# Performance work log

Measured on AMD Instinct MI355X. Metric: run time of the kernel, lower is better.

## Reference

```python
import jax, jax.numpy as jnp
import numpy as np

DIM = 1024
NUM_HEADS = 16
HEAD_DIM = DIM // NUM_HEADS


def setup_inputs() -> dict:
    key = jax.random.key(0)
    ks = jax.random.split(key, 9)
    s = 1.0 / np.sqrt(DIM)
    x = jax.random.normal(ks[0], (2, 2048, DIM), dtype=jnp.float32)
    Wq = jax.random.uniform(ks[1], (DIM, DIM), jnp.float32, -s, s)
    bq = jax.random.uniform(ks[2], (DIM,), jnp.float32, -s, s)
    Wk = jax.random.uniform(ks[3], (DIM, DIM), jnp.float32, -s, s)
    bk = jax.random.uniform(ks[4], (DIM,), jnp.float32, -s, s)
    Wv = jax.random.uniform(ks[5], (DIM, DIM), jnp.float32, -s, s)
    bv = jax.random.uniform(ks[6], (DIM,), jnp.float32, -s, s)
    Wo = jax.random.uniform(ks[7], (DIM, DIM), jnp.float32, -s, s)
    bo = jax.random.uniform(ks[8], (DIM,), jnp.float32, -s, s)
    return {"x": x, "Wq": Wq, "bq": bq, "Wk": Wk, "bk": bk,
            "Wv": Wv, "bv": bv, "Wo": Wo, "bo": bo}


def reference(x, Wq, bq, Wk, bk, Wv, bv, Wo, bo):
    B, S, _ = x.shape
    # projections (torch Linear: y = x @ W.T + b); split heads -> [B, H, S, Dh]
    def split(y):
        return y.reshape(B, S, NUM_HEADS, HEAD_DIM).transpose(0, 2, 1, 3)
    q = split(x @ Wq.T + bq)
    k = split(x @ Wk.T + bk)
    v = split(x @ Wv.T + bv)
    scale = 1.0 / np.sqrt(HEAD_DIM).astype(np.float32)
    scores = jnp.einsum('bhqd,bhkd->bhqk', q, k) * scale  # [B,H,S,S]
    attn = jax.nn.softmax(scores, axis=-1)
    ctx = jnp.einsum('bhqk,bhkd->bhqd', attn, v)  # [B,H,S,Dh]
    ctx = ctx.transpose(0, 2, 1, 3).reshape(B, S, DIM)
    return ctx @ Wo.T + bo
```

## Files before the change

kernel.cpp:

```cpp
#include <hip/hip_runtime.h>
#include <hip/hip_bf16.h>
#include <math.h>

#define DIMSZ 1024
#define NHEAD 16
#define HDIM 64
#define BATCH 2
#define SEQ 2048
#define NROWS (BATCH * SEQ)

#define QSCALE 0.18033688011112042592f

typedef __attribute__((ext_vector_type(8))) _Float16 f16x8;
typedef __attribute__((ext_vector_type(4))) float f32x4;

__device__ __forceinline__ int swz(int m) { return (m ^ (m >> 2)) & 3; }

__device__ __forceinline__ ushort f2h(float x) {
    union { _Float16 h; ushort u; } cv;
    cv.h = (_Float16)x;
    return cv.u;
}

__device__ __forceinline__ void gld16(const void* g, void* l) {
    __builtin_amdgcn_global_load_lds((const __attribute__((address_space(1))) void*)g,
                                     (__attribute__((address_space(3))) void*)l,
                                     16, 0, 0);
}

__global__ __launch_bounds__(256) void convert_all(
    const float* __restrict__ x,
    const float* __restrict__ Wq, const float* __restrict__ Wk,
    const float* __restrict__ Wv, const float* __restrict__ Wo,
    ushort* __restrict__ Xh, ushort* __restrict__ Wh, ushort* __restrict__ Woh)
{
    const int b = blockIdx.x;
    const float* src;
    ushort* dst;
    size_t off;
    if (b < 2048)      { src = x;  dst = Xh;             off = (size_t)b * 2048; }
    else if (b < 2560) { src = Wq; dst = Wh;             off = (size_t)(b - 2048) * 2048; }
    else if (b < 3072) { src = Wk; dst = Wh + (1 << 20); off = (size_t)(b - 2560) * 2048; }
    else if (b < 3584) { src = Wv; dst = Wh + 2 * (1 << 20); off = (size_t)(b - 3072) * 2048; }
    else               { src = Wo; dst = Woh;            off = (size_t)(b - 3584) * 2048; }

    const size_t i = off + (size_t)threadIdx.x * 8;
    const float4 f0 = *(const float4*)&src[i];
    const float4 f1 = *(const float4*)&src[i + 4];
    uint4 hv;
    hv.x = (unsigned)f2h(f0.x) | ((unsigned)f2h(f0.y) << 16);
    hv.y = (unsigned)f2h(f0.z) | ((unsigned)f2h(f0.w) << 16);
    hv.z = (unsigned)f2h(f1.x) | ((unsigned)f2h(f1.y) << 16);
    hv.w = (unsigned)f2h(f1.z) | ((unsigned)f2h(f1.w) << 16);
    *(uint4*)&dst[i] = hv;
}

__global__ __launch_bounds__(256, 3) void qkv_gemm(
    const ushort* __restrict__ Xh,
    const ushort* __restrict__ Wh,
    const float* __restrict__ bq, const float* __restrict__ bk,
    const float* __restrict__ bv,
    ushort* __restrict__ Qb, ushort* __restrict__ Kb, ushort* __restrict__ Vt)
{
    __shared__ __align__(16) ushort smem[17408];

    const int tid = threadIdx.x;
    const int wave = tid >> 6;
    const int lane = tid & 63;
    const int lm = lane & 15;
    const int lq = lane >> 4;
    const int wy = wave >> 1;
    const int wx = wave & 1;
    const int m0 = blockIdx.x * 128;
    const int nbase = blockIdx.y * 128;

    const int c = tid & 3;
    const int r0 = tid >> 2;
    const int g = c ^ swz(r0 & 15);
    const ushort* gah = Xh + (size_t)(m0 + r0) * DIMSZ + g * 8;
    const ushort* gbh = Wh + (size_t)(nbase + r0) * DIMSZ + g * 8;
    const int wofs = wave * 512;

    const int fo = lm * 32 + (((lq ^ swz(lm)) & 3) << 3);
    int aofs[4], bofs[4];
#pragma unroll
    for (int i = 0; i < 4; ++i) {
        aofs[i] = (wy * 64 + i * 16) * 32 + fo;
        bofs[i] = (wx * 64 + i * 16) * 32 + fo;
    }

    f32x4 acc[4][4] = {};

    {
        gld16(gah, smem + wofs);                 gld16(gah + 64 * DIMSZ, smem + 2048 + wofs);
        gld16(gbh, smem + 4096 + wofs);          gld16(gbh + 64 * DIMSZ, smem + 6144 + wofs);
    }

    for (int kk = 0; kk < 32; ++kk) {
        __syncthreads();

        const ushort* Ah = smem;
        const ushort* Bh = smem + 4096;

        f16x8 ahf[4], bhf[4];
#pragma unroll
        for (int i = 0; i < 4; ++i) {
            ahf[i] = *(const f16x8*)&Ah[aofs[i]];
            bhf[i] = *(const f16x8*)&Bh[bofs[i]];
        }

        __syncthreads();

        if (kk + 1 < 32) {
            const int k0 = (kk + 1) * 32;
            gld16(gah + k0, smem + wofs);                 gld16(gah + 64 * DIMSZ + k0, smem + 2048 + wofs);
            gld16(gbh + k0, smem + 4096 + wofs);          gld16(gbh + 64 * DIMSZ + k0, smem + 6144 + wofs);
        }

#pragma unroll
        for (int i = 0; i < 4; ++i)
#pragma unroll
            for (int j = 0; j < 4; ++j)
                acc[i][j] = __builtin_amdgcn_mfma_f32_16x16x32_f16(ahf[i], bhf[j], acc[i][j], 0, 0, 0);
    }

    const int mat = blockIdx.y >> 3;
    const float* bias = (mat == 0) ? bq : (mat == 1) ? bk : bv;
    const int nloc0 = (blockIdx.y & 7) * 128;
    const int b = m0 >> 11;
    const int s0 = m0 & (SEQ - 1);
    ushort* sf = smem;

    __syncthreads();

    if (mat == 2) {
#pragma unroll
        for (int j = 0; j < 4; ++j) {
            const int nc = nloc0 + wx * 64 + j * 16 + lm;
            const float bb = bias[nc];
            const int d = j * 16 + lm;
#pragma unroll
            for (int i = 0; i < 4; ++i) {
                const int ss = wy * 64 + (i >> 1) * 32 + lq * 8 + (i & 1) * 4;
                ushort4 pk;
                pk.x = f2h(acc[i][j][0] + bb);
                pk.y = f2h(acc[i][j][1] + bb);
                pk.z = f2h(acc[i][j][2] + bb);
                pk.w = f2h(acc[i][j][3] + bb);
                *(ushort4*)&sf[(wx * 64 + d) * 136 + ss] = pk;
            }
        }
        __syncthreads();
#pragma unroll
        for (int p = 0; p < 8; ++p) {
            const int idx = p * 256 + tid;
            const int row = idx >> 4;
            const int hh = row >> 6;
            const int d = row & 63;
            const int sseg = (idx & 15) * 8;
            const uint4 v = *(const uint4*)&sf[row * 136 + sseg];
            const int hg = (nloc0 >> 6) + hh;
            *(uint4*)&Vt[((size_t)(b * NHEAD + hg) * HDIM + d) * SEQ + s0 + sseg] = v;
        }
    } else {
        ushort* dst = (mat == 0) ? Qb : Kb;
        const float sc = (mat == 0) ? QSCALE : 1.0f;
#pragma unroll
        for (int j = 0; j < 4; ++j) {
            const int col = wx * 64 + j * 16 + lm;
            const float bb = bias[nloc0 + col];
#pragma unroll
            for (int i = 0; i < 4; ++i) {
                const int rbase = wy * 64 + i * 16 + lq * 4;
#pragma unroll
                for (int rr = 0; rr < 4; ++rr)
                    sf[(rbase + rr) * 136 + col] = f2h((acc[i][j][rr] + bb) * sc);
            }
        }
        __syncthreads();
#pragma unroll
        for (int p = 0; p < 8; ++p) {
            const int idx = p * 256 + tid;
            const int row = idx >> 4;
            const int seg = idx & 15;
            const uint4 v = *(const uint4*)&sf[row * 136 + seg * 8];
            const int nc0 = nloc0 + seg * 8;
            const int h = nc0 >> 6;
            const int d = nc0 & 63;
            *(uint4*)&dst[((size_t)(b * NHEAD + h) * SEQ + s0 + row) * HDIM + d] = v;
        }
    }
}

__global__ __launch_bounds__(512, 4) void flash_attn_mfma(
    const ushort* __restrict__ Qb, const ushort* __restrict__ Kb,
    const ushort* __restrict__ Vt, ushort* __restrict__ CTXh)
{
    __shared__ __align__(16) ushort Ks[2][4096];
    __shared__ __align__(16) ushort Vs[2][4096];

    const int tid = threadIdx.x;
    const int w = tid >> 6;
    const int l = tid & 63;
    const int lm = l & 15;
    const int lq = l >> 4;
    const int q0 = blockIdx.x * 128;
    const int bh = blockIdx.y;

    const ushort* Kg = Kb + (size_t)bh * SEQ * HDIM;
    const ushort* Vg = Vt + (size_t)bh * HDIM * SEQ;

    const int srow = w * 8 + (l >> 3);
    const int sc_ = (l & 7) ^ ((l >> 3) & 7);

    f16x8 qf[2];
#pragma unroll
    for (int kt = 0; kt < 2; ++kt)
        qf[kt] = *(const f16x8*)&Qb[((size_t)bh * SEQ + q0 + w * 16 + lm) * HDIM + kt * 32 + lq * 8];

    int koff[4][2];
#pragma unroll
    for (int t = 0; t < 4; ++t)
#pragma unroll
        for (int kt = 0; kt < 2; ++kt)
            koff[t][kt] = (t * 16 + lm) * 64 + (((kt * 4 + lq) ^ (lm & 7)) << 3);

    f32x4 o[4] = {};
    float l_ = 0.0f;

    gld16(Kg + (size_t)srow * HDIM + sc_ * 8, &Ks[0][0] + w * 8 * 64);
    gld16(Vg + (size_t)srow * SEQ + sc_ * 8, &Vs[0][0] + w * 8 * 64);

    for (int ch = 0; ch < SEQ / 64; ++ch) {
        __syncthreads();

        if (ch + 1 < SEQ / 64) {
            const int kc = (ch + 1) * 64;
            ushort* kb_n = &Ks[(ch + 1) & 1][0];
            ushort* vb_n = &Vs[(ch + 1) & 1][0];
            gld16(Kg + (size_t)(kc + srow) * HDIM + sc_ * 8, kb_n + w * 8 * 64);
            gld16(Vg + (size_t)srow * SEQ + kc + sc_ * 8, vb_n + w * 8 * 64);
        }

        const ushort* kb = &Ks[ch & 1][0];
        const ushort* vb = &Vs[ch & 1][0];

        f32x4 st[4] = {};
#pragma unroll
        for (int ct = 0; ct < 4; ++ct)
#pragma unroll
            for (int kt = 0; kt < 2; ++kt) {
                const f16x8 kf = *(const f16x8*)&kb[koff[ct][kt]];
                st[ct] = __builtin_amdgcn_mfma_f32_16x16x32_f16(kf, qf[kt], st[ct], 0, 0, 0);
            }

        {
            float ls = 0.0f;
#pragma unroll
            for (int ct = 0; ct < 4; ++ct)
#pragma unroll
                for (int r = 0; r < 4; ++r) {
                    const float p = __builtin_amdgcn_exp2f(st[ct][r]);
                    st[ct][r] = p;
                    ls += p;
                }
            ls += __shfl_xor(ls, 16, 64);
            ls += __shfl_xor(ls, 32, 64);
            l_ += ls;
        }

        f16x8 pf[2];
#pragma unroll
        for (int kt2 = 0; kt2 < 2; ++kt2) {
            union { f16x8 v; ushort u[8]; } pk;
#pragma unroll
            for (int t = 0; t < 2; ++t)
#pragma unroll
                for (int r = 0; r < 4; ++r)
                    pk.u[t * 4 + r] = f2h(st[kt2 * 2 + t][r]);
            pf[kt2] = pk.v;
        }

#pragma unroll
        for (int dt = 0; dt < 4; ++dt)
#pragma unroll
            for (int kt2 = 0; kt2 < 2; ++kt2) {
                const f16x8 vf = *(const f16x8*)&vb[koff[dt][kt2]];
                o[dt] = __builtin_amdgcn_mfma_f32_16x16x32_f16(pf[kt2], vf, o[dt], 0, 0, 0);
            }
    }

    const int b = bh >> 4;
    const int h = bh & 15;
    const float linv_me = 1.0f / l_;
#pragma unroll
    for (int r = 0; r < 4; ++r) {
        const float lr = __shfl(linv_me, lq * 4 + r, 64);
        const int srow_ = q0 + w * 16 + lq * 4 + r;
        const size_t base = ((size_t)b * SEQ + srow_) * DIMSZ + h * HDIM;
#pragma unroll
        for (int dt = 0; dt < 4; ++dt)
            CTXh[base + dt * 16 + lm] = f2h(o[dt][r] * lr);
    }
}

__global__ __launch_bounds__(256) void oproj_gemm(
    const ushort* __restrict__ Ah_g, const ushort* __restrict__ Bh_g,
    const float* __restrict__ bias, float* __restrict__ out)
{
    __shared__ __align__(16) ushort smem[6144];

    const int tid = threadIdx.x;
    const int wave = tid >> 6;
    const int lane = tid & 63;
    const int lm = lane & 15;
    const int lq = lane >> 4;
    const int wy = wave >> 1;
    const int wx = wave & 1;
    const int m0 = blockIdx.x * 64;
    const int n0 = blockIdx.y * 128;

    const int c = tid & 3;
    const int r0 = tid >> 2;
    const int g = c ^ swz(r0 & 15);
    const ushort* gah = Ah_g + (size_t)(m0 + r0) * DIMSZ + g * 8;
    const ushort* gbh = Bh_g + (size_t)(n0 + r0) * DIMSZ + g * 8;
    const int wofs = wave * 512;

    const int fo = lm * 32 + (((lq ^ swz(lm)) & 3) << 3);
    int aofs[2], bofs[4];
#pragma unroll
    for (int i = 0; i < 2; ++i) aofs[i] = (wy * 32 + i * 16) * 32 + fo;
#pragma unroll
    for (int j = 0; j < 4; ++j) bofs[j] = (wx * 64 + j * 16) * 32 + fo;

    f32x4 acc[2][4] = {};

    {
        gld16(gah, smem + wofs);
        gld16(gbh, smem + 2048 + wofs);   gld16(gbh + 64 * DIMSZ, smem + 4096 + wofs);
    }

    for (int kk = 0; kk < 32; ++kk) {
        __syncthreads();

        f16x8 ahf[2], bhf[4];
#pragma unroll
        for (int i = 0; i < 2; ++i) ahf[i] = *(const f16x8*)&smem[aofs[i]];
#pragma unroll
        for (int j = 0; j < 4; ++j) bhf[j] = *(const f16x8*)&smem[2048 + bofs[j]];

        __syncthreads();

        if (kk + 1 < 32) {
            const int k0 = (kk + 1) * 32;
            gld16(gah + k0, smem + wofs);
            gld16(gbh + k0, smem + 2048 + wofs);   gld16(gbh + 64 * DIMSZ + k0, smem + 4096 + wofs);
        }

#pragma unroll
        for (int i = 0; i < 2; ++i)
#pragma unroll
            for (int j = 0; j < 4; ++j)
                acc[i][j] = __builtin_amdgcn_mfma_f32_16x16x32_f16(ahf[i], bhf[j], acc[i][j], 0, 0, 0);
    }

#pragma unroll
    for (int j = 0; j < 4; ++j) {
        const int nc = n0 + wx * 64 + j * 16 + lm;
        const float bb = bias[nc];
#pragma unroll
        for (int i = 0; i < 2; ++i) {
            const int mb = m0 + wy * 32 + i * 16 + lq * 4;
#pragma unroll
            for (int rr = 0; rr < 4; ++rr)
                out[(size_t)(mb + rr) * DIMSZ + nc] = acc[i][j][rr] + bb;
        }
    }
}

extern "C" void kernel_launch(void* const* d_in, const int* in_sizes, int n_in,
                              void* d_out, int out_size, void* d_ws, size_t ws_size,
                              hipStream_t stream)
{
    const float* x  = (const float*)d_in[0];
    const float* Wq = (const float*)d_in[1];
    const float* bq = (const float*)d_in[2];
    const float* Wk = (const float*)d_in[3];
    const float* bk = (const float*)d_in[4];
    const float* Wv = (const float*)d_in[5];
    const float* bv = (const float*)d_in[6];
    const float* Wo = (const float*)d_in[7];
    const float* bo = (const float*)d_in[8];
    float* out = (float*)d_out;

    const size_t elems = (size_t)NROWS * DIMSZ;
    ushort* Qb   = (ushort*)d_ws;
    ushort* Kb   = Qb + elems;
    ushort* Vt   = Kb + elems;
    ushort* CTXh = Vt + elems;
    ushort* Wh   = CTXh + elems;
    ushort* Woh  = Wh + 3 * (1 << 20);
    ushort* Xh   = CTXh;

    convert_all<<<4096, 256, 0, stream>>>(x, Wq, Wk, Wv, Wo, Xh, Wh, Woh);

    qkv_gemm<<<dim3(32, 24), 256, 0, stream>>>(Xh, Wh, bq, bk, bv, Qb, Kb, Vt);

    flash_attn_mfma<<<dim3(SEQ / 128, BATCH * NHEAD), 512, 0, stream>>>(Qb, Kb, Vt, CTXh);

    oproj_gemm<<<dim3(64, 8), 256, 0, stream>>>(CTXh, Woh, bo, out);
}
```

Before: 182.4 us.

## Double KV chunk to 128, compute softmax denominator via MFMA, use packed cvt

The flash attention kernel now processes 128-key chunks per iteration instead of 64, which halves the number of barriers and loop iterations, and doubles the LDS buffers. The row-sum of probabilities is computed with an MFMA against a ones vector rather than with per-lane adds and cross-lane shuffles. Float-to-half conversion uses the packed round-toward-zero convert. This trades higher LDS use (64KB per block), which may limit occupancy under the 4-blocks launch bound, for fewer synchronisations and less VALU work. Round-toward-zero slightly changes rounding, and the denominator is now summed from the fp16-rounded probabilities.

```diff
diff --git a/kernel.cpp b/kernel.cpp
--- a/kernel.cpp
+++ b/kernel.cpp
@@ -12,6 +12,7 @@
 #define QSCALE 0.18033688011112042592f
 
 typedef __attribute__((ext_vector_type(8))) _Float16 f16x8;
+typedef __attribute__((ext_vector_type(2))) __fp16 fp16x2;
 typedef __attribute__((ext_vector_type(4))) float f32x4;
 
 __device__ __forceinline__ int swz(int m) { return (m ^ (m >> 2)) & 3; }
@@ -20,6 +21,12 @@
     union { _Float16 h; ushort u; } cv;
     cv.h = (_Float16)x;
     return cv.u;
+}
+
+__device__ __forceinline__ unsigned pkrtz(float a, float b) {
+    union { fp16x2 v; unsigned u; } c;
+    c.v = __builtin_amdgcn_cvt_pkrtz(a, b);
+    return c.u;
 }
 
 __device__ __forceinline__ void gld16(const void* g, void* l) {
@@ -196,8 +203,8 @@
     const ushort* __restrict__ Qb, const ushort* __restrict__ Kb,
     const ushort* __restrict__ Vt, ushort* __restrict__ CTXh)
 {
-    __shared__ __align__(16) ushort Ks[2][4096];
-    __shared__ __align__(16) ushort Vs[2][4096];
+    __shared__ __align__(16) ushort Ks[2][8192];
+    __shared__ __align__(16) ushort Vs[2][8192];
 
     const int tid = threadIdx.x;
     const int w = tid >> 6;
@@ -210,92 +217,99 @@
     const ushort* Kg = Kb + (size_t)bh * SEQ * HDIM;
     const ushort* Vg = Vt + (size_t)bh * HDIM * SEQ;
 
-    const int srow = w * 8 + (l >> 3);
-    const int sc_ = (l & 7) ^ ((l >> 3) & 7);
+    const int krow_ = w * 8 + (l >> 3);
+    const int kg_ = (l & 7) ^ ((l >> 3) & 7);
+    const int vrow_ = w * 4 + (l >> 4);
+    const int vg_ = (l & 15) ^ (vrow_ & 7);
 
     f16x8 qf[2];
 #pragma unroll
     for (int kt = 0; kt < 2; ++kt)
         qf[kt] = *(const f16x8*)&Qb[((size_t)bh * SEQ + q0 + w * 16 + lm) * HDIM + kt * 32 + lq * 8];
 
-    int koff[4][2];
-#pragma unroll
-    for (int t = 0; t < 4; ++t)
-#pragma unroll
-        for (int kt = 0; kt < 2; ++kt)
-            koff[t][kt] = (t * 16 + lm) * 64 + (((kt * 4 + lq) ^ (lm & 7)) << 3);
+    int kbase[2], vbase[4];
+#pragma unroll
+    for (int kt = 0; kt < 2; ++kt)
+        kbase[kt] = lm * 64 + (((kt * 4 + lq) ^ (lm & 7)) << 3);
+#pragma unroll
+    for (int kt2 = 0; kt2 < 4; ++kt2)
+        vbase[kt2] = lm * 128 + (((kt2 * 4 + lq) ^ (lm & 7)) << 3);
+
+    f16x8 vones;
+#pragma unroll
+    for (int i = 0; i < 8; ++i) vones[i] = (_Float16)1.0f;
 
     f32x4 o[4] = {};
-    float l_ = 0.0f;
-
-    gld16(Kg + (size_t)srow * HDIM + sc_ * 8, &Ks[0][0] + w * 8 * 64);
-    gld16(Vg + (size_t)srow * SEQ + sc_ * 8, &Vs[0][0] + w * 8 * 64);
-
-    for (int ch = 0; ch < SEQ / 64; ++ch) {
-        __syncthreads();
-
-        if (ch + 1 < SEQ / 64) {
-            const int kc = (ch + 1) * 64;
+    f32x4 lacc = {};
+
+#pragma unroll
+    for (int p = 0; p < 2; ++p) {
+        gld16(Kg + (size_t)(p * 64 + krow_) * HDIM + kg_ * 8, &Ks[0][0] + (p * 64 + w * 8) * 64);
+        gld16(Vg + (size_t)(p * 32 + vrow_) * SEQ + vg_ * 8, &Vs[0][0] + (p * 32 + w * 4) * 128);
+    }
+
+    for (int ch = 0; ch < SEQ / 128; ++ch) {
+        __syncthreads();
+
+        if (ch + 1 < SEQ / 128) {
+            const int kc = (ch + 1) * 128;
             ushort* kb_n = &Ks[(ch + 1) & 1][0];
             ushort* vb_n = &Vs[(ch + 1) & 1][0];
-            gld16(Kg + (size_t)(kc + srow) * HDIM + sc_ * 8, kb_n + w * 8 * 64);
-            gld16(Vg + (size_t)srow * SEQ + kc + sc_ * 8, vb_n + w * 8 * 64);
+#pragma unroll
+            for (int p = 0; p < 2; ++p) {
+                gld16(Kg + (size_t)(kc + p * 64 + krow_) * HDIM + kg_ * 8, kb_n + (p * 64 + w * 8) * 64);
+                gld16(Vg + (size_t)(p * 32 + vrow_) * SEQ + kc + vg_ * 8, vb_n + (p * 32 + w * 4) * 128);
+            }
         }
 
         const ushort* kb = &Ks[ch & 1][0];
         const ushort* vb = &Vs[ch & 1][0];
 
-        f32x4 st[4] = {};
-#pragma unroll
-        for (int ct = 0; ct < 4; ++ct)
+        f32x4 st[8] = {};
+#pragma unroll
+        for (int ct = 0; ct < 8; ++ct)
 #pragma unroll
             for (int kt = 0; kt < 2; ++kt) {
-                const f16x8 kf = *(const f16x8*)&kb[koff[ct][kt]];
+                const f16x8 kf = *(const f16x8*)&kb[ct * 1024 + kbase[kt]];
                 st[ct] = __builtin_amdgcn_mfma_f32_16x16x32_f16(kf, qf[kt], st[ct], 0, 0, 0);
             }
 
-        {
-            float ls = 0.0f;
-#pragma unroll
-            for (int ct = 0; ct < 4; ++ct)
-#pragma unroll
-                for (int r = 0; r < 4; ++r) {
-                    const float p = __builtin_amdgcn_exp2f(st[ct][r]);
-                    st[ct][r] = p;
-                    ls += p;
-                }
-            ls += __shfl_xor(ls, 16, 64);
-            ls += __shfl_xor(ls, 32, 64);
-            l_ += ls;
-        }
-
-        f16x8 pf[2];
-#pragma unroll
-        for (int kt2 = 0; kt2 < 2; ++kt2) {
-            union { f16x8 v; ushort u[8]; } pk;
-#pragma unroll
-            for (int t = 0; t < 2; ++t)
-#pragma unroll
-                for (int r = 0; r < 4; ++r)
-                    pk.u[t * 4 + r] = f2h(st[kt2 * 2 + t][r]);
+#pragma unroll
+        for (int ct = 0; ct < 8; ++ct)
+#pragma unroll
+            for (int r = 0; r < 4; ++r)
+                st[ct][r] = __builtin_amdgcn_exp2f(st[ct][r]);
+
+        f16x8 pf[4];
+#pragma unroll
+        for (int kt2 = 0; kt2 < 4; ++kt2) {
+            union { f16x8 v; unsigned u[4]; } pk;
+#pragma unroll
+            for (int t = 0; t < 2; ++t) {
+                pk.u[t * 2 + 0] = pkrtz(st[kt2 * 2 + t][0], st[kt2 * 2 + t][1]);
+                pk.u[t * 2 + 1] = pkrtz(st[kt2 * 2 + t][2], st[kt2 * 2 + t][3]);
+            }
             pf[kt2] = pk.v;
         }
 
 #pragma unroll
+        for (int kt2 = 0; kt2 < 4; ++kt2)
+            lacc = __builtin_amdgcn_mfma_f32_16x16x32_f16(pf[kt2], vones, lacc, 0, 0, 0);
+
+#pragma unroll
         for (int dt = 0; dt < 4; ++dt)
 #pragma unroll
-            for (int kt2 = 0; kt2 < 2; ++kt2) {
-                const f16x8 vf = *(const f16x8*)&vb[koff[dt][kt2]];
+            for (int kt2 = 0; kt2 < 4; ++kt2) {
+                const f16x8 vf = *(const f16x8*)&vb[dt * 2048 + vbase[kt2]];
                 o[dt] = __builtin_amdgcn_mfma_f32_16x16x32_f16(pf[kt2], vf, o[dt], 0, 0, 0);
             }
     }
 
     const int b = bh >> 4;
     const int h = bh & 15;
-    const float linv_me = 1.0f / l_;
 #pragma unroll
     for (int r = 0; r < 4; ++r) {
-        const float lr = __shfl(linv_me, lq * 4 + r, 64);
+        const float lr = 1.0f / lacc[r];
         const int srow_ = q0 + w * 16 + lq * 4 + r;
         const size_t base = ((size_t)b * SEQ + srow_) * DIMSZ + h * HDIM;
 #pragma unroll
```

Result: no change. 185.7 us (+1.8%).
